# Kernel tuning notes

Measured on AMD Instinct MI355X. Metric: run time of the kernel, lower is better.

The kernel has to match this reference:

```python
import jax, jax.numpy as jnp
import numpy as np

MASK_WEIGHT = 1.0
HEAD_DIM = 64
SCALING = HEAD_DIM ** -0.5


def _rotate_half(x):
    x1, x2 = jnp.split(x, 2, axis=-1)
    return jnp.concatenate([-x2, x1], axis=-1)


def _rope_tables(seq_len, dim, dtype):
    inv_freq = 1.0 / (10000.0 ** (jnp.arange(0, dim, 2, dtype=jnp.float32) / dim))
    t = jnp.arange(seq_len, dtype=jnp.float32)
    freqs = jnp.outer(t, inv_freq)                      # (s, d/2)
    cos = jnp.tile(jnp.cos(freqs), (1, 2)).astype(dtype)  # (s, d)  '(2 d)' tiling
    sin = jnp.tile(jnp.sin(freqs), (1, 2)).astype(dtype)
    return cos, sin


def _apply_rope(x, cos, sin):
    # x: (b, h, s, d); cos/sin: (s, d) broadcast over b, h
    return x * cos + _rotate_half(x) * sin


def setup_inputs() -> dict:
    key = jax.random.key(0)
    ks = jax.random.split(key, 6)
    b, h, s, d = 2, 16, 2048, 64
    d_model = h * d
    return {
        "q": jax.random.normal(ks[0], (b, h, s, d), jnp.float32),
        "k": jax.random.normal(ks[1], (b, h, s, d), jnp.float32),
        "v": jax.random.normal(ks[2], (b, h, s, d), jnp.float32),
        "attention_mask": jax.random.normal(ks[3], (1, h, s, s), jnp.float32) * 0.05,
        "out_w": jax.random.normal(ks[4], (d_model, d_model), jnp.float32) * (d_model ** -0.5),
        "out_b": jax.random.normal(ks[5], (d_model,), jnp.float32) * 0.02,
    }


def reference(q, k, v, attention_mask, out_w, out_b):
    b, h, s, d = q.shape
    cos, sin = _rope_tables(s, d, q.dtype)
    qr = _apply_rope(q, cos, sin)
    kr = _apply_rope(k, cos, sin)
    # learned per-head affinity transform of the queries: q' = (mask_weight * W) @ q
    W = attention_mask[0] * MASK_WEIGHT                    # (h, s, s), shared over batch
    qt = jnp.einsum('hqk,bhkd->bhqd', W, qr)
    # flash-style online softmax over keys == plain stable softmax (same math)
    scores = jnp.einsum('bhqd,bhkd->bhqk', qt, kr) * SCALING
    attn = jax.nn.softmax(scores, axis=-1)
    ctx = jnp.einsum('bhqk,bhkd->bhqd', attn, v)
    ctx = ctx.transpose(0, 2, 1, 3).reshape(b, s, h * d)   # (b, s, d_model)
    return ctx @ out_w.T + out_b
```

## Files before the change

### kernel.cpp

```cpp
#include <hip/hip_runtime.h>
#include <hip/hip_bf16.h>
#include <math.h>

typedef __bf16 bf16_t;
typedef __bf16 bf16x4 __attribute__((ext_vector_type(4)));
typedef __bf16 bf16x8 __attribute__((ext_vector_type(8)));
typedef float f32x4 __attribute__((ext_vector_type(4)));

#define NB 2
#define NH 16
#define SEQ 2048
#define HD 64
#define DMODEL 1024
#define QK_SCALE 0.125f
#define LOG2E 1.44269504088896340f
#define INV_2PI 0.15915494309189535f

__device__ __forceinline__ bf16_t to_bf16(float x) { return (bf16_t)x; }
#define MFMA16 __builtin_amdgcn_mfma_f32_16x16x32_bf16

__global__ __launch_bounds__(256) void k1_rope_pack(
    const float* __restrict__ q, const float* __restrict__ k, const float* __restrict__ v,
    bf16_t* __restrict__ qrT, bf16_t* __restrict__ krN, bf16_t* __restrict__ vT)
{
  __shared__ bf16_t tile[64][65];
  const int tid = threadIdx.x;
  const int blk = blockIdx.x;
  const int st = blk & 31;
  const int bh = blk >> 5;
  const int s0 = st * 64;

  const size_t base_sd = ((size_t)bh * SEQ + s0) * HD;
  const float* qb = q + base_sd;
  const float* kb = k + base_sd;
  const float* vb = v + base_sd;
  bf16_t* qrTb = qrT + (size_t)bh * HD * SEQ;
  bf16_t* krNb = krN + base_sd;
  bf16_t* vTb  = vT  + (size_t)bh * HD * SEQ;

  #pragma unroll
  for (int pp = 0; pp < 8; ++pp) {
    int idx = pp * 256 + tid;
    int sr = idx >> 5;
    int j  = idx & 31;
    float freq = __builtin_amdgcn_exp2f(-(float)j * (13.287712379549449f / 32.0f));
    float ang = (float)(s0 + sr) * freq;
    float rev = ang * INV_2PI;
    rev = rev - floorf(rev);
    float c  = __builtin_amdgcn_cosf(rev);
    float sn = __builtin_amdgcn_sinf(rev);
    float q1 = qb[sr*HD + j], q2 = qb[sr*HD + j + 32];
    tile[sr][j]      = to_bf16((q1*c - q2*sn) * QK_SCALE);
    tile[sr][j + 32] = to_bf16((q2*c + q1*sn) * QK_SCALE);
    float ka = kb[sr*HD + j], kbv = kb[sr*HD + j + 32];
    krNb[sr*HD + j]      = to_bf16(ka*c - kbv*sn);
    krNb[sr*HD + j + 32] = to_bf16(kbv*c + ka*sn);
  }
  __syncthreads();
  #pragma unroll
  for (int c = 0; c < 2; ++c) {
    int id = c*256 + tid;
    int d = id >> 3;
    int sc = (id & 7) * 8;
    bf16x8 vec;
    #pragma unroll
    for (int i = 0; i < 8; ++i) vec[i] = tile[sc + i][d];
    *(bf16x8*)&qrTb[(size_t)d * SEQ + s0 + sc] = vec;
  }
  __syncthreads();
  #pragma unroll
  for (int c = 0; c < 4; ++c) {
    int id = c*256 + tid;
    int sr = id >> 4;
    int c4 = (id & 15) * 4;
    float4 v4 = *(const float4*)&vb[sr*HD + c4];
    tile[sr][c4+0] = to_bf16(v4.x);
    tile[sr][c4+1] = to_bf16(v4.y);
    tile[sr][c4+2] = to_bf16(v4.z);
    tile[sr][c4+3] = to_bf16(v4.w);
  }
  __syncthreads();
  #pragma unroll
  for (int c = 0; c < 2; ++c) {
    int id = c*256 + tid;
    int d = id >> 3;
    int sc = (id & 7) * 8;
    bf16x8 vec;
    #pragma unroll
    for (int i = 0; i < 8; ++i) vec[i] = tile[sc + i][d];
    *(bf16x8*)&vTb[(size_t)d * SEQ + s0 + sc] = vec;
  }
}

__global__ __launch_bounds__(256) void k2_qt_gemm(
    const float* __restrict__ Wm,
    const bf16_t* __restrict__ qrT,
    bf16_t* __restrict__ qtT)
{
  __shared__ __align__(16) bf16_t A_lds[2][64*72];
  __shared__ __align__(16) bf16_t B_lds[64*72];
  const int tid = threadIdx.x;
  const int blk = blockIdx.x;
  const int n0 = (blk & 31) * 64;
  const int h = blk >> 5;
  const int wave = tid >> 6, lane = tid & 63;
  const int l15 = lane & 15, quad = lane >> 4;
  const int rs = tid >> 2, cs = (tid & 3) * 16;

  const float* Wh = Wm + (size_t)h * SEQ * SEQ + (size_t)n0 * SEQ;
  const bf16_t* A0 = qrT + ((size_t)h * HD + rs) * SEQ;
  const bf16_t* A1 = qrT + (((size_t)NH + h) * HD + rs) * SEQ;

  f32x4 acc[2][4] = {};
  float4 wreg[4];
  bf16x8 areg[2][2];

  #pragma unroll
  for (int i = 0; i < 4; ++i) wreg[i] = *(const float4*)&Wh[(size_t)rs*SEQ + cs + i*4];
  #pragma unroll
  for (int i = 0; i < 2; ++i) {
    areg[0][i] = *(const bf16x8*)&A0[cs + i*8];
    areg[1][i] = *(const bf16x8*)&A1[cs + i*8];
  }

  for (int it = 0; it < SEQ/64; ++it) {
    if (it) __syncthreads();
    #pragma unroll
    for (int i = 0; i < 2; ++i) {
      *(bf16x8*)&A_lds[0][rs*72 + cs + i*8] = areg[0][i];
      *(bf16x8*)&A_lds[1][rs*72 + cs + i*8] = areg[1][i];
      bf16x8 wb;
      float4 wa = wreg[i*2], wc = wreg[i*2+1];
      wb[0]=to_bf16(wa.x); wb[1]=to_bf16(wa.y); wb[2]=to_bf16(wa.z); wb[3]=to_bf16(wa.w);
      wb[4]=to_bf16(wc.x); wb[5]=to_bf16(wc.y); wb[6]=to_bf16(wc.z); wb[7]=to_bf16(wc.w);
      *(bf16x8*)&B_lds[rs*72 + cs + i*8] = wb;
    }
    __syncthreads();
    if (it + 1 < SEQ/64) {
      int kb = (it + 1) * 64;
      #pragma unroll
      for (int i = 0; i < 4; ++i) wreg[i] = *(const float4*)&Wh[(size_t)rs*SEQ + kb + cs + i*4];
      #pragma unroll
      for (int i = 0; i < 2; ++i) {
        areg[0][i] = *(const bf16x8*)&A0[kb + cs + i*8];
        areg[1][i] = *(const bf16x8*)&A1[kb + cs + i*8];
      }
    }
    #pragma unroll
    for (int kc = 0; kc < 2; ++kc) {
      const int off = kc*32 + quad*8;
      bf16x8 bfr[4];
      #pragma unroll
      for (int nt = 0; nt < 4; ++nt)
        bfr[nt] = *(const bf16x8*)&B_lds[(nt*16 + l15)*72 + off];
      #pragma unroll
      for (int b2 = 0; b2 < 2; ++b2) {
        bf16x8 af = *(const bf16x8*)&A_lds[b2][(wave*16 + l15)*72 + off];
        #pragma unroll
        for (int nt = 0; nt < 4; ++nt)
          acc[b2][nt] = MFMA16(af, bfr[nt], acc[b2][nt], 0, 0, 0);
      }
    }
  }
  #pragma unroll
  for (int b2 = 0; b2 < 2; ++b2)
    #pragma unroll
    for (int nt = 0; nt < 4; ++nt)
      #pragma unroll
      for (int r = 0; r < 4; ++r) {
        int d = wave*16 + quad*4 + r;
        qtT[(((size_t)b2*NH + h)*HD + d)*SEQ + n0 + nt*16 + l15] =
            to_bf16(acc[b2][nt][r] * LOG2E);
      }
}

__global__ __launch_bounds__(256, 2) void k3_flash(
    const bf16_t* __restrict__ qtT,
    const bf16_t* __restrict__ krN,
    const bf16_t* __restrict__ vT,
    bf16_t* __restrict__ ctx)
{
  __shared__ __align__(16) bf16_t K_lds[64*72];
  __shared__ __align__(16) bf16_t V_lds[64*72];
  __shared__ __align__(16) bf16_t P_lds[4][16*72];
  const int tid = threadIdx.x;
  const int blk = blockIdx.x;
  const int qt = blk & 15;
  const int bh = blk >> 4;
  const int h = bh & 15, b = bh >> 4;
  const int wave = tid >> 6, lane = tid & 63;
  const int l15 = lane & 15, quad = lane >> 4;
  const int qw = qt*128 + wave*32;
  const int srow = tid >> 3, sch = (tid & 7) * 8;

  const bf16_t* qtb = qtT + (size_t)bh * HD * SEQ;
  const bf16_t* krb = krN + (size_t)bh * SEQ * HD;
  const bf16_t* vtb = vT  + (size_t)bh * HD * SEQ;

  bf16x8 Qf[2][2];
  #pragma unroll
  for (int g = 0; g < 2; ++g)
    #pragma unroll
    for (int c = 0; c < 2; ++c)
      #pragma unroll
      for (int j = 0; j < 8; ++j)
        Qf[g][c][j] = qtb[(size_t)(c*32 + quad*8 + j)*SEQ + qw + g*16 + l15];

  bf16x8 ones;
  #pragma unroll
  for (int j = 0; j < 8; ++j) ones[j] = to_bf16(1.0f);

  f32x4 O[2][4] = {};
  f32x4 L[2] = {};

  bf16x8 kreg[2], vreg[2];
  #pragma unroll
  for (int c = 0; c < 2; ++c) {
    int row = c*32 + srow;
    kreg[c] = *(const bf16x8*)&krb[(size_t)row*HD + sch];
    vreg[c] = *(const bf16x8*)&vtb[(size_t)row*SEQ + sch];
  }

  for (int kt = 0; kt < 32; ++kt) {
    if (kt) __syncthreads();
    #pragma unroll
    for (int c = 0; c < 2; ++c) {
      int row = c*32 + srow;
      *(bf16x8*)&K_lds[row*72 + sch] = kreg[c];
      *(bf16x8*)&V_lds[row*72 + sch] = vreg[c];
    }
    __syncthreads();
    if (kt + 1 < 32) {
      #pragma unroll
      for (int c = 0; c < 2; ++c) {
        int row = c*32 + srow;
        kreg[c] = *(const bf16x8*)&krb[(size_t)((kt+1)*64 + row)*HD + sch];
        vreg[c] = *(const bf16x8*)&vtb[(size_t)row*SEQ + (kt+1)*64 + sch];
      }
    }

    bf16x8 ak[4][2], bv[4][2];
    #pragma unroll
    for (int nt = 0; nt < 4; ++nt) {
      ak[nt][0] = *(const bf16x8*)&K_lds[(nt*16 + l15)*72 + quad*8];
      ak[nt][1] = *(const bf16x8*)&K_lds[(nt*16 + l15)*72 + 32 + quad*8];
      bv[nt][0] = *(const bf16x8*)&V_lds[(nt*16 + l15)*72 + quad*8];
      bv[nt][1] = *(const bf16x8*)&V_lds[(nt*16 + l15)*72 + 32 + quad*8];
    }

    #pragma unroll
    for (int g = 0; g < 2; ++g) {
      f32x4 s[4] = {};
      #pragma unroll
      for (int nt = 0; nt < 4; ++nt) {
        s[nt] = MFMA16(ak[nt][0], Qf[g][0], s[nt], 0, 0, 0);
        s[nt] = MFMA16(ak[nt][1], Qf[g][1], s[nt], 0, 0, 0);
      }
      #pragma unroll
      for (int nt = 0; nt < 4; ++nt) {
        bf16x4 pk;
        #pragma unroll
        for (int r = 0; r < 4; ++r)
          pk[r] = to_bf16(__builtin_amdgcn_exp2f(s[nt][r]));
        *(bf16x4*)&P_lds[wave][l15*72 + nt*16 + quad*4] = pk;
      }
      bf16x8 ap0 = *(const bf16x8*)&P_lds[wave][l15*72 + quad*8];
      bf16x8 ap1 = *(const bf16x8*)&P_lds[wave][l15*72 + 32 + quad*8];
      #pragma unroll
      for (int nt = 0; nt < 4; ++nt) {
        O[g][nt] = MFMA16(ap0, bv[nt][0], O[g][nt], 0, 0, 0);
        O[g][nt] = MFMA16(ap1, bv[nt][1], O[g][nt], 0, 0, 0);
      }
      L[g] = MFMA16(ap0, ones, L[g], 0, 0, 0);
      L[g] = MFMA16(ap1, ones, L[g], 0, 0, 0);
    }
  }

  #pragma unroll
  for (int g = 0; g < 2; ++g)
    #pragma unroll
    for (int nt = 0; nt < 4; ++nt)
      #pragma unroll
      for (int r = 0; r < 4; ++r) {
        int qrow = qw + g*16 + quad*4 + r;
        float o = O[g][nt][r] / L[g][r];
        ctx[((size_t)b*SEQ + qrow)*DMODEL + h*HD + nt*16 + l15] = to_bf16(o);
      }
}

__global__ __launch_bounds__(256) void k4_proj(
    const bf16_t* __restrict__ ctx,
    const float* __restrict__ w,
    const float* __restrict__ bias,
    float* __restrict__ out)
{
  __shared__ __align__(16) bf16_t A_lds[128*72];
  __shared__ __align__(16) bf16_t B_lds[64*72];
  const int tid = threadIdx.x;
  const int blk = blockIdx.x;
  const int n0 = (blk & 15) * 64;
  const int m0 = (blk >> 4) * 128;
  const int wave = tid >> 6, lane = tid & 63;
  const int l15 = lane & 15, quad = lane >> 4;
  const int ra = tid >> 1, ca = (tid & 1) * 32;
  const int rs = tid >> 2, cs = (tid & 3) * 16;

  f32x4 acc[2][4] = {};
  bf16x8 areg[4];
  float4 wreg[4];

  #pragma unroll
  for (int i = 0; i < 4; ++i) {
    areg[i] = *(const bf16x8*)&ctx[(size_t)(m0 + ra)*DMODEL + ca + i*8];
    wreg[i] = *(const float4*)&w[(size_t)(n0 + rs)*DMODEL + cs + i*4];
  }

  for (int it = 0; it < DMODEL/64; ++it) {
    if (it) __syncthreads();
    #pragma unroll
    for (int i = 0; i < 4; ++i)
      *(bf16x8*)&A_lds[ra*72 + ca + i*8] = areg[i];
    #pragma unroll
    for (int i = 0; i < 2; ++i) {
      bf16x8 wb;
      float4 wa = wreg[i*2], wc = wreg[i*2+1];
      wb[0]=to_bf16(wa.x); wb[1]=to_bf16(wa.y); wb[2]=to_bf16(wa.z); wb[3]=to_bf16(wa.w);
      wb[4]=to_bf16(wc.x); wb[5]=to_bf16(wc.y); wb[6]=to_bf16(wc.z); wb[7]=to_bf16(wc.w);
      *(bf16x8*)&B_lds[rs*72 + cs + i*8] = wb;
    }
    __syncthreads();
    if (it + 1 < DMODEL/64) {
      int kb = (it + 1) * 64;
      #pragma unroll
      for (int i = 0; i < 4; ++i) {
        areg[i] = *(const bf16x8*)&ctx[(size_t)(m0 + ra)*DMODEL + kb + ca + i*8];
        wreg[i] = *(const float4*)&w[(size_t)(n0 + rs)*DMODEL + kb + cs + i*4];
      }
    }
    #pragma unroll
    for (int kc = 0; kc < 2; ++kc) {
      const int off = kc*32 + quad*8;
      bf16x8 bfr[4];
      #pragma unroll
      for (int nt = 0; nt < 4; ++nt)
        bfr[nt] = *(const bf16x8*)&B_lds[(nt*16 + l15)*72 + off];
      #pragma unroll
      for (int g = 0; g < 2; ++g) {
        bf16x8 af = *(const bf16x8*)&A_lds[(wave*32 + g*16 + l15)*72 + off];
        #pragma unroll
        for (int nt = 0; nt < 4; ++nt)
          acc[g][nt] = MFMA16(af, bfr[nt], acc[g][nt], 0, 0, 0);
      }
    }
  }
  #pragma unroll
  for (int nt = 0; nt < 4; ++nt) {
    float bb = bias[n0 + nt*16 + l15];
    #pragma unroll
    for (int g = 0; g < 2; ++g)
      #pragma unroll
      for (int r = 0; r < 4; ++r)
        out[(size_t)(m0 + wave*32 + g*16 + quad*4 + r)*DMODEL + n0 + nt*16 + l15] =
            acc[g][nt][r] + bb;
  }
}

extern "C" void kernel_launch(void* const* d_in, const int* in_sizes, int n_in,
                              void* d_out, int out_size, void* d_ws, size_t ws_size,
                              hipStream_t stream)
{
  const float* q     = (const float*)d_in[0];
  const float* k     = (const float*)d_in[1];
  const float* v     = (const float*)d_in[2];
  const float* mask  = (const float*)d_in[3];
  const float* out_w = (const float*)d_in[4];
  const float* out_b = (const float*)d_in[5];
  float* out = (float*)d_out;

  const size_t elems = (size_t)NB * NH * SEQ * HD;
  bf16_t* qrT = (bf16_t*)d_ws;
  bf16_t* krN = qrT + elems;
  bf16_t* vT  = krN + elems;
  bf16_t* qtT = vT  + elems;
  bf16_t* ctx = qtT + elems;

  k1_rope_pack<<<dim3(NB*NH*(SEQ/64)), dim3(256), 0, stream>>>(q, k, v, qrT, krN, vT);
  k2_qt_gemm <<<dim3(NH*(SEQ/64)),     dim3(256), 0, stream>>>(mask, qrT, qtT);
  k3_flash   <<<dim3(NB*NH*(SEQ/128)), dim3(256), 0, stream>>>(qtT, krN, vT, ctx);
  k4_proj    <<<dim3((NB*SEQ/128)*(DMODEL/64)), dim3(256), 0, stream>>>(ctx, out_w, out_b, out);
}
```

Measured before the change: 497.4 us.

## Vectorize RoPE loads/stores, remap block order for XCDs, add MFMA priority hints

```diff
diff --git a/kernel.cpp b/kernel.cpp
--- a/kernel.cpp
+++ b/kernel.cpp
@@ -39,22 +39,35 @@
   bf16_t* vTb  = vT  + (size_t)bh * HD * SEQ;
 
   #pragma unroll
-  for (int pp = 0; pp < 8; ++pp) {
+  for (int pp = 0; pp < 2; ++pp) {
     int idx = pp * 256 + tid;
-    int sr = idx >> 5;
-    int j  = idx & 31;
-    float freq = __builtin_amdgcn_exp2f(-(float)j * (13.287712379549449f / 32.0f));
-    float ang = (float)(s0 + sr) * freq;
-    float rev = ang * INV_2PI;
-    rev = rev - floorf(rev);
-    float c  = __builtin_amdgcn_cosf(rev);
-    float sn = __builtin_amdgcn_sinf(rev);
-    float q1 = qb[sr*HD + j], q2 = qb[sr*HD + j + 32];
-    tile[sr][j]      = to_bf16((q1*c - q2*sn) * QK_SCALE);
-    tile[sr][j + 32] = to_bf16((q2*c + q1*sn) * QK_SCALE);
-    float ka = kb[sr*HD + j], kbv = kb[sr*HD + j + 32];
-    krNb[sr*HD + j]      = to_bf16(ka*c - kbv*sn);
-    krNb[sr*HD + j + 32] = to_bf16(kbv*c + ka*sn);
+    int sr = idx >> 3;
+    int j0 = (idx & 7) * 4;
+    float4 q1 = *(const float4*)&qb[sr*HD + j0];
+    float4 q2 = *(const float4*)&qb[sr*HD + j0 + 32];
+    float4 ka = *(const float4*)&kb[sr*HD + j0];
+    float4 kc = *(const float4*)&kb[sr*HD + j0 + 32];
+    float q1a[4] = {q1.x, q1.y, q1.z, q1.w};
+    float q2a[4] = {q2.x, q2.y, q2.z, q2.w};
+    float kaa[4] = {ka.x, ka.y, ka.z, ka.w};
+    float kca[4] = {kc.x, kc.y, kc.z, kc.w};
+    bf16x4 kr1, kr2;
+    #pragma unroll
+    for (int t = 0; t < 4; ++t) {
+      int j = j0 + t;
+      float freq = __builtin_amdgcn_exp2f(-(float)j * (13.287712379549449f / 32.0f));
+      float ang = (float)(s0 + sr) * freq;
+      float rev = ang * INV_2PI;
+      rev = rev - floorf(rev);
+      float c  = __builtin_amdgcn_cosf(rev);
+      float sn = __builtin_amdgcn_sinf(rev);
+      tile[sr][j]      = to_bf16((q1a[t]*c - q2a[t]*sn) * QK_SCALE);
+      tile[sr][j + 32] = to_bf16((q2a[t]*c + q1a[t]*sn) * QK_SCALE);
+      kr1[t] = to_bf16(kaa[t]*c - kca[t]*sn);
+      kr2[t] = to_bf16(kca[t]*c + kaa[t]*sn);
+    }
+    *(bf16x4*)&krNb[sr*HD + j0]      = kr1;
+    *(bf16x4*)&krNb[sr*HD + j0 + 32] = kr2;
   }
   __syncthreads();
   #pragma unroll
@@ -100,7 +113,7 @@
   __shared__ __align__(16) bf16_t A_lds[2][64*72];
   __shared__ __align__(16) bf16_t B_lds[64*72];
   const int tid = threadIdx.x;
-  const int blk = blockIdx.x;
+  const int blk = (blockIdx.x & 7) * 64 + (blockIdx.x >> 3);
   const int n0 = (blk & 31) * 64;
   const int h = blk >> 5;
   const int wave = tid >> 6, lane = tid & 63;
@@ -184,7 +197,7 @@
   __shared__ __align__(16) bf16_t V_lds[64*72];
   __shared__ __align__(16) bf16_t P_lds[4][16*72];
   const int tid = threadIdx.x;
-  const int blk = blockIdx.x;
+  const int blk = (blockIdx.x & 7) * 64 + (blockIdx.x >> 3);
   const int qt = blk & 15;
   const int bh = blk >> 4;
   const int h = bh & 15, b = bh >> 4;
@@ -251,11 +264,13 @@
     #pragma unroll
     for (int g = 0; g < 2; ++g) {
       f32x4 s[4] = {};
+      __builtin_amdgcn_s_setprio(1);
       #pragma unroll
       for (int nt = 0; nt < 4; ++nt) {
         s[nt] = MFMA16(ak[nt][0], Qf[g][0], s[nt], 0, 0, 0);
         s[nt] = MFMA16(ak[nt][1], Qf[g][1], s[nt], 0, 0, 0);
       }
+      __builtin_amdgcn_s_setprio(0);
       #pragma unroll
       for (int nt = 0; nt < 4; ++nt) {
         bf16x4 pk;
@@ -266,6 +281,7 @@
       }
       bf16x8 ap0 = *(const bf16x8*)&P_lds[wave][l15*72 + quad*8];
       bf16x8 ap1 = *(const bf16x8*)&P_lds[wave][l15*72 + 32 + quad*8];
+      __builtin_amdgcn_s_setprio(1);
       #pragma unroll
       for (int nt = 0; nt < 4; ++nt) {
         O[g][nt] = MFMA16(ap0, bv[nt][0], O[g][nt], 0, 0, 0);
@@ -273,6 +289,7 @@
       }
       L[g] = MFMA16(ap0, ones, L[g], 0, 0, 0);
       L[g] = MFMA16(ap1, ones, L[g], 0, 0, 0);
+      __builtin_amdgcn_s_setprio(0);
     }
   }
 
```

Result: no change. 492.9 us (-0.9%).
